# Kernel tuning notes

Hardware: AMD Instinct MI355X
Metric: run time of the kernel (lower is better)

Reference implementation:

```python
import jax, jax.numpy as jnp
import numpy as np

N_NODES = 100000
N_EDGES = 1600000
HID = 128
HEADS = 8
DK = HID // HEADS
N_LAYERS = 4
IN_DIM = 32
N_CLASSES = 16


def _ln(x, g, b, eps=1e-5):
    mu = x.mean(-1, keepdims=True)
    var = x.var(-1, keepdims=True)
    return (x - mu) / jnp.sqrt(var + eps) * g + b


def setup_inputs() -> dict:
    key = jax.random.key(0)
    ks = jax.random.split(key, 24)
    s = 0.05
    inp = {
        'feat': jax.random.randint(ks[0], (N_NODES,), 0, IN_DIM, dtype=jnp.int32),
        'edge_src': jax.random.randint(ks[1], (N_EDGES,), 0, N_NODES, dtype=jnp.int32),
        'edge_dst': jnp.sort(jax.random.randint(ks[2], (N_EDGES,), 0, N_NODES, dtype=jnp.int32)),
        'emb': jax.random.normal(ks[3], (IN_DIM, HID), jnp.float32) * s,
        'Wq': jax.random.normal(ks[4], (N_LAYERS, HID, HID), jnp.float32) * s,
        'Wk': jax.random.normal(ks[5], (N_LAYERS, HID, HID), jnp.float32) * s,
        'Wv': jax.random.normal(ks[6], (N_LAYERS, HID, HID), jnp.float32) * s,
        'Wo': jax.random.normal(ks[7], (N_LAYERS, HID, HID), jnp.float32) * s,
        'bo': jnp.zeros((N_LAYERS, HID), jnp.float32),
        'ln1_g': jnp.ones((N_LAYERS, HID), jnp.float32),
        'ln1_b': jnp.zeros((N_LAYERS, HID), jnp.float32),
        'W1': jax.random.normal(ks[8], (N_LAYERS, HID, 2 * HID), jnp.float32) * s,
        'b1': jnp.zeros((N_LAYERS, 2 * HID), jnp.float32),
        'W2': jax.random.normal(ks[9], (N_LAYERS, 2 * HID, HID), jnp.float32) * s,
        'b2': jnp.zeros((N_LAYERS, HID), jnp.float32),
        'ln2_g': jnp.ones((N_LAYERS, HID), jnp.float32),
        'ln2_b': jnp.zeros((N_LAYERS, HID), jnp.float32),
        'mW0': jax.random.normal(ks[10], (HID, HID // 2), jnp.float32) * s,
        'mb0': jnp.zeros((HID // 2,), jnp.float32),
        'mW1': jax.random.normal(ks[11], (HID // 2, HID // 4), jnp.float32) * s,
        'mb1': jnp.zeros((HID // 4,), jnp.float32),
        'mW2': jax.random.normal(ks[12], (HID // 4, N_CLASSES), jnp.float32) * s,
        'mb2': jnp.zeros((N_CLASSES,), jnp.float32),
    }
    return inp


def reference(feat, edge_src, edge_dst, emb, Wq, Wk, Wv, Wo, bo, ln1_g, ln1_b,
              W1, b1, W2, b2, ln2_g, ln2_b, mW0, mb0, mW1, mb1, mW2, mb2):
    N = feat.shape[0]
    h = emb[feat]  # [N, HID] embedding gather
    inv_sqrt_dk = jnp.float32(1.0 / np.sqrt(DK))
    for l in range(Wq.shape[0]):
        h_in1 = h
        q = (h @ Wq[l]).reshape(N, HEADS, DK)
        k = (h @ Wk[l]).reshape(N, HEADS, DK)
        v = (h @ Wv[l]).reshape(N, HEADS, DK)
        # per-edge scores: K[src] . Q[dst], scaled, clipped, exponentiated
        sc = jnp.einsum('ehd,ehd->eh', k[edge_src], q[edge_dst]) * inv_sqrt_dk
        sc = jnp.exp(jnp.clip(sc, -5.0, 5.0))  # [E, HEADS]
        wV = jax.ops.segment_sum(sc[:, :, None] * v[edge_src], edge_dst, num_segments=N)
        z = jax.ops.segment_sum(sc, edge_dst, num_segments=N)
        attn = (wV / (z[:, :, None] + 1e-6)).reshape(N, HID)
        h = h_in1 + (attn @ Wo[l] + bo[l])  # residual + O proj
        h = _ln(h, ln1_g[l], ln1_b[l])
        h_in2 = h
        f = jax.nn.relu(h @ W1[l] + b1[l]) @ W2[l] + b2[l]
        h = _ln(h_in2 + f, ln2_g[l], ln2_b[l])
    # MLPReadout: HID -> HID/2 -> HID/4 -> n_classes
    h = jax.nn.relu(h @ mW0 + mb0)
    h = jax.nn.relu(h @ mW1 + mb1)
    return h @ mW2 + mb2
```

## Files before the change

kernel.cpp:

```cpp
#include <hip/hip_runtime.h>
#include <hip/hip_fp16.h>

#define HID 128
#define N_LAYERS 4
#define IN_DIM 32
#define N_CLASSES 16

typedef _Float16 f16x8 __attribute__((ext_vector_type(8)));
typedef float f32x2 __attribute__((ext_vector_type(2)));
typedef __attribute__((ext_vector_type(4))) float f32x4;
typedef unsigned int uint_t;

#if defined(__has_builtin)
#if __has_builtin(__builtin_amdgcn_cvt_pk_f32_fp8)
#define HAVE_CVT_FP8 1
#endif
#if __has_builtin(__builtin_amdgcn_cvt_pk_fp8_f32)
#define HAVE_ENC_FP8 1
#endif
#endif

__device__ __forceinline__ unsigned short f2bf(float f) {
    unsigned int u = __float_as_uint(f);
    return (unsigned short)((u + 0x7FFFu + ((u >> 16) & 1u)) >> 16);
}
__device__ __forceinline__ float2 up16(uint_t u) {
    __half2 h = *(__half2*)&u;
    return __half22float2(h);
}

__device__ __forceinline__ unsigned char f2e4m3(float f) {
    unsigned int u = __float_as_uint(f);
    unsigned char s = (unsigned char)((u >> 24) & 0x80u);
    unsigned int a = u & 0x7FFFFFFFu;
    if (a >= 0x43E00000u) return s | 0x7Eu;
    int exp = (int)(a >> 23) - 127;
    if (exp < -6) {
        int m = (int)rintf(__uint_as_float(a) * 512.f);
        return s | (unsigned char)m;
    }
    unsigned int lsb = (a >> 20) & 1u;
    a += 0x7FFFFu + lsb;
    int e8 = ((int)(a >> 23) - 127) + 7;
    unsigned int m8 = (a >> 20) & 7u;
    return s | (unsigned char)((e8 << 3) | (int)m8);
}
__device__ __forceinline__ float e4m32f(unsigned int b) {
    unsigned int s = (b & 0x80u) << 24;
    unsigned int E = (b >> 3) & 15u, m = b & 7u;
    if (E == 0) {
        float v = (float)m * 0.001953125f;
        return __uint_as_float(__float_as_uint(v) | s);
    }
    return __uint_as_float(s | ((E + 120u) << 23) | (m << 20));
}
__device__ __forceinline__ unsigned char enc8(float v) {
#ifdef HAVE_ENC_FP8
    int r = __builtin_amdgcn_cvt_pk_fp8_f32(v, v, 0, false);
    return (unsigned char)(r & 0xFF);
#else
    return f2e4m3(v);
#endif
}
__device__ __forceinline__ void dec8v(uint_t u, f32x2* o) {
#ifdef HAVE_CVT_FP8
    o[0] = __builtin_amdgcn_cvt_pk_f32_fp8(u, false);
    o[1] = __builtin_amdgcn_cvt_pk_f32_fp8(u, true);
#else
    o[0] = (f32x2){e4m32f(u & 255u), e4m32f((u >> 8) & 255u)};
    o[1] = (f32x2){e4m32f((u >> 16) & 255u), e4m32f(u >> 24)};
#endif
}

__global__ void detect_kernel(const unsigned int* __restrict__ ln1g, int* __restrict__ flag) {
    if (threadIdx.x == 0 && blockIdx.x == 0)
        *flag = (ln1g[0] == 0x3F800000u) ? 0 : 1;
}

#define NSM 11
struct SArgs {
    const void* src[NSM];
    float*      dst[NSM];
    int         cnt[NSM];
};

__global__ void conv_kernel(SArgs args, const int* __restrict__ flag) {
    int p = blockIdx.y;
    int n = args.cnt[p];
    int base = (blockIdx.x * 256 + threadIdx.x) * 4;
    if (base >= n) return;
    float* dst = args.dst[p];
    if (*flag) {
        const unsigned short* s = (const unsigned short*)args.src[p];
        #pragma unroll
        for (int j = 0; j < 4; ++j)
            dst[base + j] = __uint_as_float(((unsigned int)s[base + j]) << 16);
    } else {
        const float* s = (const float*)args.src[p];
        *(float4*)&dst[base] = *(const float4*)&s[base];
    }
}

#define NW 27
struct WArgs {
    const void* src[NW];
    int         soff[NW];
    _Float16*   dst[NW];
    int         K[NW];
    int         M[NW];
};

__global__ void wconv_kernel(WArgs a, const int* __restrict__ flag) {
    int p = blockIdx.y;
    int K = a.K[p], M = a.M[p];
    int idx = blockIdx.x * 256 + threadIdx.x;
    if (idx >= K * M) return;
    int k = idx / M, m = idx % M;
    float v;
    if (*flag)
        v = __uint_as_float(((unsigned int)((const unsigned short*)a.src[p])[a.soff[p] + idx]) << 16);
    else
        v = ((const float*)a.src[p])[a.soff[p] + idx];
    a.dst[p][(size_t)m * K + k] = (_Float16)v;
}

__global__ void csr_kernel(const int* __restrict__ dst, int* __restrict__ row_start,
                           int N, int E) {
    int n = blockIdx.x * 256 + threadIdx.x;
    if (n > N) return;
    int lo = 0, hi = E;
    while (lo < hi) {
        int mid = (lo + hi) >> 1;
        if (dst[mid] < n) lo = mid + 1; else hi = mid;
    }
    row_start[n] = lo;
}

__global__ void embed_kernel(const int* __restrict__ feat, const float* __restrict__ emb,
                             _Float16* __restrict__ h, int N) {
    int idx = blockIdx.x * 256 + threadIdx.x;
    if (idx >= N * 16) return;
    int n  = idx >> 4;
    int c8 = idx & 15;
    int f = feat[n];
    const float* s = &emb[(size_t)f * HID + c8 * 8];
    float4 a = *(const float4*)s;
    float4 b = *(const float4*)(s + 4);
    f16x8 o;
    o[0] = (_Float16)a.x; o[1] = (_Float16)a.y; o[2] = (_Float16)a.z; o[3] = (_Float16)a.w;
    o[4] = (_Float16)b.x; o[5] = (_Float16)b.y; o[6] = (_Float16)b.z; o[7] = (_Float16)b.w;
    *(f16x8*)&h[(size_t)n * HID + c8 * 8] = o;
}

template<int K, int KC, int MC>
__launch_bounds__(256)
__global__ void mfma_gemm_qkv(const _Float16* __restrict__ Ain,
                              const _Float16* __restrict__ Bt,
                              _Float16* __restrict__ q16, unsigned char* __restrict__ kvp8) {
    constexpr int NT  = MC / 16;
    constexpr int SAB = KC * 2 + 16;

    __shared__ __align__(16) char As[64 * SAB];
    __shared__ __align__(16) char Bs[MC * SAB];

    const int t    = threadIdx.x;
    const int w    = t >> 6;
    const int l    = t & 63;
    const int quad = l >> 4;
    const int lc   = l & 15;
    const int row0 = blockIdx.x * 64;
    const int mbase = blockIdx.y * MC;

    f32x4 acc[NT];
    #pragma unroll
    for (int i = 0; i < NT; ++i) acc[i] = (f32x4){0.f, 0.f, 0.f, 0.f};

    {
        constexpr int AU = 64 * KC / 8;
        #pragma unroll
        for (int i = 0; i < (AU + 255) / 256; ++i) {
            int idx = t + i * 256;
            if ((AU % 256 == 0) || idx < AU) {
                int r = idx / (KC / 8), u = idx % (KC / 8);
                *(uint4*)&As[r * SAB + u * 16] =
                    *(const uint4*)(Ain + (size_t)(row0 + r) * K + u * 8);
            }
        }
        constexpr int BU = MC * KC / 8;
        #pragma unroll
        for (int i = 0; i < (BU + 255) / 256; ++i) {
            int idx = t + i * 256;
            if ((BU % 256 == 0) || idx < BU) {
                int m = idx / (KC / 8), u = idx % (KC / 8);
                *(uint4*)&Bs[m * SAB + u * 16] =
                    *(const uint4*)(Bt + (size_t)(mbase + m) * K + u * 8);
            }
        }
        __syncthreads();
        #pragma unroll
        for (int kk = 0; kk < KC / 32; ++kk) {
            f16x8 af = *(const f16x8*)&As[(w * 16 + lc) * SAB + kk * 64 + quad * 16];
            #pragma unroll
            for (int i = 0; i < NT; ++i) {
                f16x8 bf = *(const f16x8*)&Bs[(i * 16 + lc) * SAB + kk * 64 + quad * 16];
                acc[i] = __builtin_amdgcn_mfma_f32_16x16x32_f16(af, bf, acc[i], 0, 0, 0);
            }
        }
    }

    #pragma unroll
    for (int r = 0; r < 4; ++r) {
        int row = row0 + w * 16 + quad * 4 + r;
        #pragma unroll
        for (int i = 0; i < NT; ++i) {
            float v = acc[i][r];
            int gc = mbase + i * 16 + lc;
            if (gc < 128)      q16[(size_t)row * 128 + gc] = (_Float16)v;
            else if (gc < 256) kvp8[(size_t)row * 256 + (gc - 128)] = enc8(v);
            else               kvp8[(size_t)row * 256 + 128 + (gc - 256)] = enc8(v);
        }
    }
}

template<int NEXTM, bool RMODE>
__launch_bounds__(256)
__global__ void layer_tail_fused(const _Float16* __restrict__ t2, _Float16* __restrict__ h,
                                 const _Float16* __restrict__ Wo, const _Float16* __restrict__ W1,
                                 const _Float16* __restrict__ W2,
                                 const _Float16* __restrict__ Wn, const float* __restrict__ bn,
                                 const float* __restrict__ bo,  const float* __restrict__ l1g,
                                 const float* __restrict__ l1b, const float* __restrict__ b1,
                                 const float* __restrict__ b2,  const float* __restrict__ l2g,
                                 const float* __restrict__ l2b,
                                 _Float16* __restrict__ q16, unsigned char* __restrict__ kvp8) {
    constexpr int SAB = 272;
    __shared__ __align__(16) char bufA[64 * SAB];
    __shared__ __align__(16) char bufT[64 * SAB];
    __shared__ __align__(16) char bufH[64 * SAB];
    __shared__ __align__(16) char bufB[64 * SAB];

    const int t    = threadIdx.x;
    const int w    = t >> 6;
    const int l    = t & 63;
    const int quad = l >> 4;
    const int lc   = l & 15;
    const int row0 = blockIdx.x * 64;
    const int arow = (w * 16 + lc) * SAB;

    #pragma unroll
    for (int i = 0; i < 4; ++i) {
        int idx = t + i * 256;
        int r = idx >> 4, u = idx & 15;
        *(uint4*)&bufA[r * SAB + u * 16] = *(const uint4*)(t2 + (size_t)(row0 + r) * 128 + u * 8);
        *(uint4*)&bufT[r * SAB + u * 16] = *(const uint4*)(h  + (size_t)(row0 + r) * 128 + u * 8);
    }

    f32x4 acc[8];
    #pragma unroll
    for (int i = 0; i < 8; ++i) acc[i] = (f32x4){0.f, 0.f, 0.f, 0.f};
    #pragma unroll
    for (int c = 0; c < 2; ++c) {
        if (c) __syncthreads();
        #pragma unroll
        for (int i = 0; i < 4; ++i) {
            int idx = t + i * 256;
            int r = idx >> 4, u = idx & 15;
            *(uint4*)&bufB[r * SAB + u * 16] = *(const uint4*)(Wo + (size_t)(c * 64 + r) * 128 + u * 8);
        }
        __syncthreads();
        #pragma unroll
        for (int kk = 0; kk < 4; ++kk) {
            f16x8 af = *(const f16x8*)&bufA[arow + kk * 64 + quad * 16];
            #pragma unroll
            for (int i = 0; i < 4; ++i) {
                f16x8 bf = *(const f16x8*)&bufB[(i * 16 + lc) * SAB + kk * 64 + quad * 16];
                acc[c * 4 + i] = __builtin_amdgcn_mfma_f32_16x16x32_f16(af, bf, acc[c * 4 + i], 0, 0, 0);
            }
        }
    }
    {
        float gv[8], bv[8], bb[8];
        #pragma unroll
        for (int j = 0; j < 8; ++j) {
            int col = j * 16 + lc;
            gv[j] = l1g[col]; bv[j] = l1b[col]; bb[j] = bo[col];
        }
        #pragma unroll
        for (int r = 0; r < 4; ++r) {
            int lrow = (w * 16 + quad * 4 + r) * SAB;
            float v[8];
            float s = 0.f, ss = 0.f;
            #pragma unroll
            for (int j = 0; j < 8; ++j) {
                float res = (float)*(const _Float16*)&bufT[lrow + (j * 16 + lc) * 2];
                v[j] = acc[j][r] + bb[j] + res;
                s += v[j]; ss += v[j] * v[j];
            }
            #pragma unroll
            for (int m = 1; m <= 8; m <<= 1) { s += __shfl_xor(s, m); ss += __shfl_xor(ss, m); }
            float mu   = s * (1.f / 128.f);
            float rstd = rsqrtf(ss * (1.f / 128.f) - mu * mu + 1e-5f);
            #pragma unroll
            for (int j = 0; j < 8; ++j) {
                float o = (v[j] - mu) * rstd * gv[j] + bv[j];
                *(_Float16*)&bufH[lrow + (j * 16 + lc) * 2] = (_Float16)o;
            }
        }
    }

    #pragma unroll
    for (int c = 0; c < 4; ++c) {
        __syncthreads();
        #pragma unroll
        for (int i = 0; i < 4; ++i) {
            int idx = t + i * 256;
            int r = idx >> 4, u = idx & 15;
            *(uint4*)&bufB[r * SAB + u * 16] = *(const uint4*)(W1 + (size_t)(c * 64 + r) * 128 + u * 8);
        }
        __syncthreads();
        f32x4 a2[4];
        #pragma unroll
        for (int i = 0; i < 4; ++i) a2[i] = (f32x4){0.f, 0.f, 0.f, 0.f};
        #pragma unroll
        for (int kk = 0; kk < 4; ++kk) {
            f16x8 af = *(const f16x8*)&bufH[arow + kk * 64 + quad * 16];
            #pragma unroll
            for (int i = 0; i < 4; ++i) {
                f16x8 bf = *(const f16x8*)&bufB[(i * 16 + lc) * SAB + kk * 64 + quad * 16];
                a2[i] = __builtin_amdgcn_mfma_f32_16x16x32_f16(af, bf, a2[i], 0, 0, 0);
            }
        }
        char* plane = (c < 2) ? bufA : bufT;
        const int cbyte = (c & 1) * 128;
        #pragma unroll
        for (int r = 0; r < 4; ++r) {
            int lrow = (w * 16 + quad * 4 + r) * SAB;
            #pragma unroll
            for (int i = 0; i < 4; ++i) {
                float v = a2[i][r] + b1[c * 64 + i * 16 + lc];
                v = fmaxf(v, 0.f);
                *(_Float16*)&plane[lrow + cbyte + (i * 16 + lc) * 2] = (_Float16)v;
            }
        }
    }

    f32x4 acc3[8];
    #pragma unroll
    for (int i = 0; i < 8; ++i) acc3[i] = (f32x4){0.f, 0.f, 0.f, 0.f};
    #pragma unroll
    for (int cc = 0; cc < 2; ++cc) {
        #pragma unroll
        for (int kh = 0; kh < 2; ++kh) {
            __syncthreads();
            #pragma unroll
            for (int i = 0; i < 4; ++i) {
                int idx = t + i * 256;
                int r = idx >> 4, u = idx & 15;
                *(uint4*)&bufB[r * SAB + u * 16] =
                    *(const uint4*)(W2 + (size_t)(cc * 64 + r) * 256 + kh * 128 + u * 8);
            }
            __syncthreads();
            const char* Ap = kh ? bufT : bufA;
            #pragma unroll
            for (int kk = 0; kk < 4; ++kk) {
                f16x8 af = *(const f16x8*)&Ap[arow + kk * 64 + quad * 16];
                #pragma unroll
                for (int i = 0; i < 4; ++i) {
                    f16x8 bf = *(const f16x8*)&bufB[(i * 16 + lc) * SAB + kk * 64 + quad * 16];
                    acc3[cc * 4 + i] = __builtin_amdgcn_mfma_f32_16x16x32_f16(af, bf, acc3[cc * 4 + i], 0, 0, 0);
                }
            }
        }
    }
    {
        float gv[8], bv[8], bb[8];
        #pragma unroll
        for (int j = 0; j < 8; ++j) {
            int col = j * 16 + lc;
            gv[j] = l2g[col]; bv[j] = l2b[col]; bb[j] = b2[col];
        }
        #pragma unroll
        for (int r = 0; r < 4; ++r) {
            int row = row0 + w * 16 + quad * 4 + r;
            int lrow = (w * 16 + quad * 4 + r) * SAB;
            float v[8];
            float s = 0.f, ss = 0.f;
            #pragma unroll
            for (int j = 0; j < 8; ++j) {
                float res = (float)*(const _Float16*)&bufH[lrow + (j * 16 + lc) * 2];
                v[j] = acc3[j][r] + bb[j] + res;
                s += v[j]; ss += v[j] * v[j];
            }
            #pragma unroll
            for (int m = 1; m <= 8; m <<= 1) { s += __shfl_xor(s, m); ss += __shfl_xor(ss, m); }
            float mu   = s * (1.f / 128.f);
            float rstd = rsqrtf(ss * (1.f / 128.f) - mu * mu + 1e-5f);
            #pragma unroll
            for (int j = 0; j < 8; ++j) {
                float o = (v[j] - mu) * rstd * gv[j] + bv[j];
                h[(size_t)row * 128 + j * 16 + lc] = (_Float16)o;
                *(_Float16*)&bufA[lrow + (j * 16 + lc) * 2] = (_Float16)o;
            }
        }
    }

    #pragma unroll
    for (int c = 0; c < NEXTM / 64; ++c) {
        __syncthreads();
        #pragma unroll
        for (int i = 0; i < 4; ++i) {
            int idx = t + i * 256;
            int r = idx >> 4, u = idx & 15;
            *(uint4*)&bufB[r * SAB + u * 16] = *(const uint4*)(Wn + (size_t)(c * 64 + r) * 128 + u * 8);
        }
        __syncthreads();
        f32x4 a4[4];
        #pragma unroll
        for (int i = 0; i < 4; ++i) a4[i] = (f32x4){0.f, 0.f, 0.f, 0.f};
        #pragma unroll
        for (int kk = 0; kk < 4; ++kk) {
            f16x8 af = *(const f16x8*)&bufA[arow + kk * 64 + quad * 16];
            #pragma unroll
            for (int i = 0; i < 4; ++i) {
                f16x8 bf = *(const f16x8*)&bufB[(i * 16 + lc) * SAB + kk * 64 + quad * 16];
                a4[i] = __builtin_amdgcn_mfma_f32_16x16x32_f16(af, bf, a4[i], 0, 0, 0);
            }
        }
        #pragma unroll
        for (int r = 0; r < 4; ++r) {
            int row = row0 + w * 16 + quad * 4 + r;
            #pragma unroll
            for (int i = 0; i < 4; ++i) {
                int gc = c * 64 + i * 16 + lc;
                float v = a4[i][r];
                if (RMODE) {
                    v += bn[gc];
                    v = fmaxf(v, 0.f);
                    q16[(size_t)row * 64 + gc] = (_Float16)v;
                } else {
                    if (gc < 128)      q16[(size_t)row * 128 + gc] = (_Float16)v;
                    else if (gc < 256) kvp8[(size_t)row * 256 + (gc - 128)] = enc8(v);
                    else               kvp8[(size_t)row * 256 + 128 + (gc - 256)] = enc8(v);
                }
            }
        }
    }
}

__launch_bounds__(256)
__global__ void readout_tail(const _Float16* __restrict__ r0,
                             const _Float16* __restrict__ w1t, const float* __restrict__ b1_,
                             const _Float16* __restrict__ w2t, const float* __restrict__ b2_,
                             void* __restrict__ outp, const int* __restrict__ flag, int N) {
    constexpr int SA = 144;
    constexpr int SR = 80;
    __shared__ __align__(16) char bufA[64 * SA];
    __shared__ __align__(16) char bufR[64 * SR];

    const int t    = threadIdx.x;
    const int w    = t >> 6;
    const int l    = t & 63;
    const int quad = l >> 4;
    const int lc   = l & 15;
    const int row0 = blockIdx.x * 64;

    #pragma unroll
    for (int i = 0; i < 2; ++i) {
        int idx = t + i * 256;
        int r = idx >> 3, u = idx & 7;
        *(uint4*)&bufA[r * SA + u * 16] = *(const uint4*)(r0 + (size_t)(row0 + r) * 64 + u * 8);
    }
    __syncthreads();

    f32x4 acc[2];
    acc[0] = (f32x4){0.f, 0.f, 0.f, 0.f};
    acc[1] = (f32x4){0.f, 0.f, 0.f, 0.f};
    #pragma unroll
    for (int kk = 0; kk < 2; ++kk) {
        f16x8 af = *(const f16x8*)&bufA[(w * 16 + lc) * SA + kk * 64 + quad * 16];
        #pragma unroll
        for (int i = 0; i < 2; ++i) {
            f16x8 bf = *(const f16x8*)(w1t + (size_t)(i * 16 + lc) * 64 + kk * 32 + quad * 8);
            acc[i] = __builtin_amdgcn_mfma_f32_16x16x32_f16(af, bf, acc[i], 0, 0, 0);
        }
    }
    #pragma unroll
    for (int r = 0; r < 4; ++r) {
        int lrow = (w * 16 + quad * 4 + r) * SR;
        #pragma unroll
        for (int i = 0; i < 2; ++i) {
            float v = acc[i][r] + b1_[i * 16 + lc];
            v = fmaxf(v, 0.f);
            *(_Float16*)&bufR[lrow + (i * 16 + lc) * 2] = (_Float16)v;
        }
    }
    f32x4 a2 = (f32x4){0.f, 0.f, 0.f, 0.f};
    {
        f16x8 af = *(const f16x8*)&bufR[(w * 16 + lc) * SR + quad * 16];
        f16x8 bf = *(const f16x8*)(w2t + (size_t)lc * 32 + quad * 8);
        a2 = __builtin_amdgcn_mfma_f32_16x16x32_f16(af, bf, a2, 0, 0, 0);
    }
    #pragma unroll
    for (int r = 0; r < 4; ++r) {
        int row = row0 + w * 16 + quad * 4 + r;
        if (row < N) {
            float v = a2[r] + b2_[lc];
            size_t o = (size_t)row * 16 + lc;
            if (*flag) ((unsigned short*)outp)[o] = f2bf(v);
            else       ((float*)outp)[o] = v;
        }
    }
}

__global__ void attn_kernel(const _Float16* __restrict__ q16, const uint_t* __restrict__ kvp,
                            const int* __restrict__ esrc, const int* __restrict__ rows,
                            _Float16* __restrict__ out, int N) {
    int node = (blockIdx.x * blockDim.x + threadIdx.x) >> 6;
    if (node >= N) return;
    int l    = threadIdx.x & 63;
    int head = l & 7;
    int eg   = l >> 3;

    f32x2 qh[8];
    {
        const uint4* qp = (const uint4*)(q16 + (size_t)node * HID + head * 16);
        uint4 q0 = qp[0], q1 = qp[1];
        uint_t qs[8] = {q0.x, q0.y, q0.z, q0.w, q1.x, q1.y, q1.z, q1.w};
        #pragma unroll
        for (int i = 0; i < 8; ++i) {
            float2 f = up16(qs[i]);
            qh[i] = (f32x2){f.x * 0.25f, f.y * 0.25f};
        }
    }
    int e0 = rows[node], e1 = rows[node + 1];
    f32x2 wv[8];
    #pragma unroll
    for (int i = 0; i < 8; ++i) wv[i] = (f32x2){0.f, 0.f};
    float z = 0.f;

    for (int eb = e0; eb < e1; eb += 16) {
        int ea = eb + eg, ec = eb + 8 + eg;
        bool oka = ea < e1, okc = ec < e1;
        int sa  = esrc[oka ? ea : e1 - 1];
        int sc_ = esrc[okc ? ec : e1 - 1];
        uint4 ka = *(const uint4*)(kvp + (size_t)sa  * 64 + head * 4);
        uint4 va = *(const uint4*)(kvp + (size_t)sa  * 64 + 32 + head * 4);
        uint4 kc = *(const uint4*)(kvp + (size_t)sc_ * 64 + head * 4);
        uint4 vc = *(const uint4*)(kvp + (size_t)sc_ * 64 + 32 + head * 4);

        f32x2 k2a[8], k2c[8];
        dec8v(ka.x, k2a); dec8v(ka.y, k2a + 2); dec8v(ka.z, k2a + 4); dec8v(ka.w, k2a + 6);
        dec8v(kc.x, k2c); dec8v(kc.y, k2c + 2); dec8v(kc.z, k2c + 4); dec8v(kc.w, k2c + 6);
        f32x2 da2 = (f32x2){0.f, 0.f}, dc2 = (f32x2){0.f, 0.f};
        #pragma unroll
        for (int j = 0; j < 8; ++j) { da2 += qh[j] * k2a[j]; dc2 += qh[j] * k2c[j]; }
        float da = da2.x + da2.y, dc = dc2.x + dc2.y;
        float sa2 = oka ? __expf(fminf(fmaxf(da, -5.f), 5.f)) : 0.f;
        float sc2 = okc ? __expf(fminf(fmaxf(dc, -5.f), 5.f)) : 0.f;

        f32x2 v2a[8], v2c[8];
        dec8v(va.x, v2a); dec8v(va.y, v2a + 2); dec8v(va.z, v2a + 4); dec8v(va.w, v2a + 6);
        dec8v(vc.x, v2c); dec8v(vc.y, v2c + 2); dec8v(vc.z, v2c + 4); dec8v(vc.w, v2c + 6);
        f32x2 pa = (f32x2){sa2, sa2}, pc = (f32x2){sc2, sc2};
        #pragma unroll
        for (int j = 0; j < 8; ++j) { wv[j] += pa * v2a[j]; wv[j] += pc * v2c[j]; }
        z += sa2 + sc2;
    }
    #pragma unroll
    for (int m = 8; m < 64; m <<= 1) {
        z += __shfl_xor(z, m);
        #pragma unroll
        for (int i = 0; i < 8; ++i) {
            wv[i].x += __shfl_xor(wv[i].x, m);
            wv[i].y += __shfl_xor(wv[i].y, m);
        }
    }
    if (eg == 0) {
        float inv = 1.f / (z + 1e-6f);
        f16x8 o0, o1;
        #pragma unroll
        for (int i = 0; i < 4; ++i) {
            o0[2*i]   = (_Float16)(wv[i].x * inv);
            o0[2*i+1] = (_Float16)(wv[i].y * inv);
            o1[2*i]   = (_Float16)(wv[4+i].x * inv);
            o1[2*i+1] = (_Float16)(wv[4+i].y * inv);
        }
        *(f16x8*)&out[(size_t)node * HID + head * 16]     = o0;
        *(f16x8*)&out[(size_t)node * HID + head * 16 + 8] = o1;
    }
}

extern "C" void kernel_launch(void* const* d_in, const int* in_sizes, int n_in,
                              void* d_out, int out_size, void* d_ws, size_t ws_size,
                              hipStream_t stream) {
    const int N  = in_sizes[0];
    const int E  = in_sizes[1];
    const int RB = (N + 63) / 64;
    const size_t NP = (size_t)RB * 64;

    const int* d_feat = (const int*)d_in[0];
    const int* d_esrc = (const int*)d_in[1];
    const int* d_edst = (const int*)d_in[2];

    char* base = (char*)d_ws;
    size_t cur = 0;
    auto alloc = [&](size_t bytes) -> char* {
        cur = (cur + 255) & ~(size_t)255;
        char* p = base + cur;
        cur += bytes;
        return p;
    };
    int* d_flag = (int*)alloc(4);
    int* d_rows = (int*)alloc((size_t)(N + 1) * 4);

    float* p_emb = (float*)alloc(IN_DIM * HID * 4);
    float* p_bo  = (float*)alloc(N_LAYERS * HID * 4);
    float* p_l1g = (float*)alloc(N_LAYERS * HID * 4);
    float* p_l1b = (float*)alloc(N_LAYERS * HID * 4);
    float* p_b1  = (float*)alloc(N_LAYERS * 2 * HID * 4);
    float* p_b2  = (float*)alloc(N_LAYERS * HID * 4);
    float* p_l2g = (float*)alloc(N_LAYERS * HID * 4);
    float* p_l2b = (float*)alloc(N_LAYERS * HID * 4);
    float* p_mb0 = (float*)alloc(64 * 4);
    float* p_mb1 = (float*)alloc(32 * 4);
    float* p_mb2 = (float*)alloc(16 * 4);

    _Float16* wqkv_t = (_Float16*)alloc((size_t)N_LAYERS * 384 * 128 * 2);
    _Float16* wo_t   = (_Float16*)alloc((size_t)N_LAYERS * 128 * 128 * 2);
    _Float16* w1_t   = (_Float16*)alloc((size_t)N_LAYERS * 256 * 128 * 2);
    _Float16* w2_t   = (_Float16*)alloc((size_t)N_LAYERS * 128 * 256 * 2);
    _Float16* mw0_t  = (_Float16*)alloc(64 * 128 * 2);
    _Float16* mw1_t  = (_Float16*)alloc(32 * 64 * 2);
    _Float16* mw2_t  = (_Float16*)alloc(16 * 32 * 2);

    _Float16*      buf_h = (_Float16*)alloc(NP * HID * 2);
    _Float16*      q16   = (_Float16*)alloc(NP * HID * 2);
    _Float16*      t2    = (_Float16*)alloc(NP * HID * 2);
    unsigned char* kvp   = (unsigned char*)alloc(NP * 256);

    detect_kernel<<<1, 64, 0, stream>>>((const unsigned int*)d_in[9], d_flag);

    {
        SArgs sa;
        const int sidx[NSM] = {3, 8, 9, 10, 12, 14, 15, 16, 18, 20, 22};
        float*    sdst[NSM] = {p_emb, p_bo, p_l1g, p_l1b, p_b1, p_b2, p_l2g, p_l2b, p_mb0, p_mb1, p_mb2};
        const int scnt[NSM] = {IN_DIM*HID, N_LAYERS*HID, N_LAYERS*HID, N_LAYERS*HID,
                               N_LAYERS*2*HID, N_LAYERS*HID, N_LAYERS*HID, N_LAYERS*HID, 64, 32, 16};
        for (int i = 0; i < NSM; ++i) { sa.src[i] = d_in[sidx[i]]; sa.dst[i] = sdst[i]; sa.cnt[i] = scnt[i]; }
        conv_kernel<<<dim3(4, NSM), 256, 0, stream>>>(sa, d_flag);
    }

    {
        WArgs wa;
        int wi = 0;
        auto addw = [&](int inp, int off, int Kd, int Md, _Float16* dst) {
            wa.src[wi] = d_in[inp]; wa.soff[wi] = off; wa.K[wi] = Kd; wa.M[wi] = Md;
            wa.dst[wi] = dst; ++wi;
        };
        for (int l = 0; l < N_LAYERS; ++l) {
            addw(4,  l * 16384, 128, 128, wqkv_t + (size_t)l * 49152);
            addw(5,  l * 16384, 128, 128, wqkv_t + (size_t)l * 49152 + 16384);
            addw(6,  l * 16384, 128, 128, wqkv_t + (size_t)l * 49152 + 32768);
            addw(7,  l * 16384, 128, 128, wo_t + (size_t)l * 16384);
            addw(11, l * 32768, 128, 256, w1_t + (size_t)l * 32768);
            addw(13, l * 32768, 256, 128, w2_t + (size_t)l * 32768);
        }
        addw(17, 0, 128, 64, mw0_t);
        addw(19, 0, 64,  32, mw1_t);
        addw(21, 0, 32,  16, mw2_t);
        wconv_kernel<<<dim3(128, NW), 256, 0, stream>>>(wa, d_flag);
    }

    csr_kernel<<<(N + 1 + 255) / 256, 256, 0, stream>>>(d_edst, d_rows, N, E);
    embed_kernel<<<((size_t)N * 16 + 255) / 256, 256, 0, stream>>>(d_feat, p_emb, buf_h, N);

    const int GBW = (N + 3) / 4;

    mfma_gemm_qkv<128, 128, 192><<<dim3(RB, 2), 256, 0, stream>>>(buf_h, wqkv_t, q16, kvp);

    for (int l = 0; l < N_LAYERS; ++l) {
        const _Float16* Wo = wo_t + (size_t)l * 16384;
        const _Float16* W1 = w1_t + (size_t)l * 32768;
        const _Float16* W2 = w2_t + (size_t)l * 32768;
        const float* bo  = p_bo  + (size_t)l * HID;
        const float* l1g = p_l1g + (size_t)l * HID;
        const float* l1b = p_l1b + (size_t)l * HID;
        const float* b1  = p_b1  + (size_t)l * 2 * HID;
        const float* b2  = p_b2  + (size_t)l * HID;
        const float* l2g = p_l2g + (size_t)l * HID;
        const float* l2b = p_l2b + (size_t)l * HID;

        attn_kernel<<<GBW, 256, 0, stream>>>(q16, (const uint_t*)kvp, d_esrc, d_rows, t2, N);

        if (l < N_LAYERS - 1) {
            layer_tail_fused<384, false><<<RB, 256, 0, stream>>>(
                t2, buf_h, Wo, W1, W2, wqkv_t + (size_t)(l + 1) * 49152, nullptr,
                bo, l1g, l1b, b1, b2, l2g, l2b, q16, kvp);
        } else {
            layer_tail_fused<64, true><<<RB, 256, 0, stream>>>(
                t2, buf_h, Wo, W1, W2, mw0_t, p_mb0,
                bo, l1g, l1b, b1, b2, l2g, l2b, q16, nullptr);
        }
    }

    readout_tail<<<RB, 256, 0, stream>>>(q16, mw1_t, p_mb1, mw2_t, p_mb2, d_out, d_flag, N);
}
```

Measured before the change: 842.6 us.

## Load GEMM B operands directly from global into registers, drop LDS weight staging

Weight tiles for the QKV GEMM and the fused layer-tail GEMMs are now read straight from global memory (L2-resident) into registers with one-tile-ahead prefetch, instead of being staged through a shared-memory buffer. This removes the bufB LDS buffer and the __syncthreads pairs around each weight load. The activation loads are reorganised so each wave fills only its own rows, and launch bounds request 3 blocks per CU. The QKV kernel becomes a single-dimension grid computing all 384 columns per block. The cost is that every wave re-reads the weights from cache, with more global traffic and register pressure.

Measured after the change: 1.335 ms. 1.58x slower.

```diff
diff --git a/kernel.cpp b/kernel.cpp
--- a/kernel.cpp
+++ b/kernel.cpp
@@ -152,78 +152,72 @@
     *(f16x8*)&h[(size_t)n * HID + c8 * 8] = o;
 }
 
-template<int K, int KC, int MC>
-__launch_bounds__(256)
+template<int NT>
+__device__ __forceinline__ void gemm128_gB(const char* Arow, const _Float16* Bt,
+                                           int colstride, int lc, int quad, f32x4* acc) {
+    uint4 cur[4], nxt[4];
+    const _Float16* p0 = Bt + (size_t)lc * colstride + quad * 8;
+    #pragma unroll
+    for (int kk = 0; kk < 4; ++kk) cur[kk] = *(const uint4*)(p0 + kk * 32);
+    #pragma unroll
+    for (int i = 0; i < NT; ++i) {
+        if (i + 1 < NT) {
+            const _Float16* p = p0 + (size_t)(i + 1) * 16 * colstride;
+            #pragma unroll
+            for (int kk = 0; kk < 4; ++kk) nxt[kk] = *(const uint4*)(p + kk * 32);
+        }
+        #pragma unroll
+        for (int kk = 0; kk < 4; ++kk) {
+            f16x8 af = *(const f16x8*)(Arow + kk * 64 + quad * 16);
+            acc[i] = __builtin_amdgcn_mfma_f32_16x16x32_f16(af, *(const f16x8*)&cur[kk],
+                                                            acc[i], 0, 0, 0);
+        }
+        #pragma unroll
+        for (int kk = 0; kk < 4; ++kk) cur[kk] = nxt[kk];
+    }
+}
+
+__launch_bounds__(256, 3)
 __global__ void mfma_gemm_qkv(const _Float16* __restrict__ Ain,
                               const _Float16* __restrict__ Bt,
                               _Float16* __restrict__ q16, unsigned char* __restrict__ kvp8) {
-    constexpr int NT  = MC / 16;
-    constexpr int SAB = KC * 2 + 16;
-
+    constexpr int SAB = 272;
     __shared__ __align__(16) char As[64 * SAB];
-    __shared__ __align__(16) char Bs[MC * SAB];
-
-    const int t    = threadIdx.x;
-    const int w    = t >> 6;
-    const int l    = t & 63;
-    const int quad = l >> 4;
-    const int lc   = l & 15;
+    const int t = threadIdx.x, w = t >> 6, l = t & 63;
+    const int quad = l >> 4, lc = l & 15;
     const int row0 = blockIdx.x * 64;
-    const int mbase = blockIdx.y * MC;
-
-    f32x4 acc[NT];
-    #pragma unroll
-    for (int i = 0; i < NT; ++i) acc[i] = (f32x4){0.f, 0.f, 0.f, 0.f};
-
-    {
-        constexpr int AU = 64 * KC / 8;
-        #pragma unroll
-        for (int i = 0; i < (AU + 255) / 256; ++i) {
-            int idx = t + i * 256;
-            if ((AU % 256 == 0) || idx < AU) {
-                int r = idx / (KC / 8), u = idx % (KC / 8);
-                *(uint4*)&As[r * SAB + u * 16] =
-                    *(const uint4*)(Ain + (size_t)(row0 + r) * K + u * 8);
+    const int arow = (w * 16 + lc) * SAB;
+
+    #pragma unroll
+    for (int i = 0; i < 4; ++i) {
+        int idx = i * 64 + l;
+        int rr = idx >> 4, u = idx & 15;
+        *(uint4*)&As[(w * 16 + rr) * SAB + u * 16] =
+            *(const uint4*)(Ain + (size_t)(row0 + w * 16 + rr) * 128 + u * 8);
+    }
+    #pragma unroll
+    for (int c = 0; c < 6; ++c) {
+        f32x4 acc[4];
+        #pragma unroll
+        for (int i = 0; i < 4; ++i) acc[i] = (f32x4){0.f, 0.f, 0.f, 0.f};
+        gemm128_gB<4>(As + arow, Bt + (size_t)c * 64 * 128, 128, lc, quad, acc);
+        #pragma unroll
+        for (int r = 0; r < 4; ++r) {
+            int row = row0 + w * 16 + quad * 4 + r;
+            #pragma unroll
+            for (int i = 0; i < 4; ++i) {
+                float v = acc[i][r];
+                int gc = c * 64 + i * 16 + lc;
+                if (gc < 128)      q16[(size_t)row * 128 + gc] = (_Float16)v;
+                else if (gc < 256) kvp8[(size_t)row * 256 + (gc - 128)] = enc8(v);
+                else               kvp8[(size_t)row * 256 + 128 + (gc - 256)] = enc8(v);
             }
         }
-        constexpr int BU = MC * KC / 8;
-        #pragma unroll
-        for (int i = 0; i < (BU + 255) / 256; ++i) {
-            int idx = t + i * 256;
-            if ((BU % 256 == 0) || idx < BU) {
-                int m = idx / (KC / 8), u = idx % (KC / 8);
-                *(uint4*)&Bs[m * SAB + u * 16] =
-                    *(const uint4*)(Bt + (size_t)(mbase + m) * K + u * 8);
-            }
-        }
-        __syncthreads();
-        #pragma unroll
-        for (int kk = 0; kk < KC / 32; ++kk) {
-            f16x8 af = *(const f16x8*)&As[(w * 16 + lc) * SAB + kk * 64 + quad * 16];
-            #pragma unroll
-            for (int i = 0; i < NT; ++i) {
-                f16x8 bf = *(const f16x8*)&Bs[(i * 16 + lc) * SAB + kk * 64 + quad * 16];
-                acc[i] = __builtin_amdgcn_mfma_f32_16x16x32_f16(af, bf, acc[i], 0, 0, 0);
-            }
-        }
-    }
-
-    #pragma unroll
-    for (int r = 0; r < 4; ++r) {
-        int row = row0 + w * 16 + quad * 4 + r;
-        #pragma unroll
-        for (int i = 0; i < NT; ++i) {
-            float v = acc[i][r];
-            int gc = mbase + i * 16 + lc;
-            if (gc < 128)      q16[(size_t)row * 128 + gc] = (_Float16)v;
-            else if (gc < 256) kvp8[(size_t)row * 256 + (gc - 128)] = enc8(v);
-            else               kvp8[(size_t)row * 256 + 128 + (gc - 256)] = enc8(v);
-        }
     }
 }
 
 template<int NEXTM, bool RMODE>
-__launch_bounds__(256)
+__launch_bounds__(256, 3)
 __global__ void layer_tail_fused(const _Float16* __restrict__ t2, _Float16* __restrict__ h,
                                  const _Float16* __restrict__ Wo, const _Float16* __restrict__ W1,
                                  const _Float16* __restrict__ W2,
@@ -237,47 +231,26 @@
     __shared__ __align__(16) char bufA[64 * SAB];
     __shared__ __align__(16) char bufT[64 * SAB];
     __shared__ __align__(16) char bufH[64 * SAB];
-    __shared__ __align__(16) char bufB[64 * SAB];
-
-    const int t    = threadIdx.x;
-    const int w    = t >> 6;
-    const int l    = t & 63;
-    const int quad = l >> 4;
-    const int lc   = l & 15;
+
+    const int t = threadIdx.x, w = t >> 6, l = t & 63;
+    const int quad = l >> 4, lc = l & 15;
     const int row0 = blockIdx.x * 64;
     const int arow = (w * 16 + lc) * SAB;
 
     #pragma unroll
     for (int i = 0; i < 4; ++i) {
-        int idx = t + i * 256;
-        int r = idx >> 4, u = idx & 15;
-        *(uint4*)&bufA[r * SAB + u * 16] = *(const uint4*)(t2 + (size_t)(row0 + r) * 128 + u * 8);
-        *(uint4*)&bufT[r * SAB + u * 16] = *(const uint4*)(h  + (size_t)(row0 + r) * 128 + u * 8);
+        int idx = i * 64 + l;
+        int rr = idx >> 4, u = idx & 15;
+        int grow = row0 + w * 16 + rr;
+        *(uint4*)&bufA[(w * 16 + rr) * SAB + u * 16] = *(const uint4*)(t2 + (size_t)grow * 128 + u * 8);
+        *(uint4*)&bufT[(w * 16 + rr) * SAB + u * 16] = *(const uint4*)(h  + (size_t)grow * 128 + u * 8);
     }
 
     f32x4 acc[8];
     #pragma unroll
     for (int i = 0; i < 8; ++i) acc[i] = (f32x4){0.f, 0.f, 0.f, 0.f};
-    #pragma unroll
-    for (int c = 0; c < 2; ++c) {
-        if (c) __syncthreads();
-        #pragma unroll
-        for (int i = 0; i < 4; ++i) {
-            int idx = t + i * 256;
-            int r = idx >> 4, u = idx & 15;
-            *(uint4*)&bufB[r * SAB + u * 16] = *(const uint4*)(Wo + (size_t)(c * 64 + r) * 128 + u * 8);
-        }
-        __syncthreads();
-        #pragma unroll
-        for (int kk = 0; kk < 4; ++kk) {
-            f16x8 af = *(const f16x8*)&bufA[arow + kk * 64 + quad * 16];
-            #pragma unroll
-            for (int i = 0; i < 4; ++i) {
-                f16x8 bf = *(const f16x8*)&bufB[(i * 16 + lc) * SAB + kk * 64 + quad * 16];
-                acc[c * 4 + i] = __builtin_amdgcn_mfma_f32_16x16x32_f16(af, bf, acc[c * 4 + i], 0, 0, 0);
-            }
-        }
-    }
+    gemm128_gB<8>(bufA + arow, Wo, 128, lc, quad, acc);
+
     {
         float gv[8], bv[8], bb[8];
         #pragma unroll
@@ -310,26 +283,10 @@
 
     #pragma unroll
     for (int c = 0; c < 4; ++c) {
-        __syncthreads();
-        #pragma unroll
-        for (int i = 0; i < 4; ++i) {
-            int idx = t + i * 256;
-            int r = idx >> 4, u = idx & 15;
-            *(uint4*)&bufB[r * SAB + u * 16] = *(const uint4*)(W1 + (size_t)(c * 64 + r) * 128 + u * 8);
-        }
-        __syncthreads();
         f32x4 a2[4];
         #pragma unroll
         for (int i = 0; i < 4; ++i) a2[i] = (f32x4){0.f, 0.f, 0.f, 0.f};
-        #pragma unroll
-        for (int kk = 0; kk < 4; ++kk) {
-            f16x8 af = *(const f16x8*)&bufH[arow + kk * 64 + quad * 16];
-            #pragma unroll
-            for (int i = 0; i < 4; ++i) {
-                f16x8 bf = *(const f16x8*)&bufB[(i * 16 + lc) * SAB + kk * 64 + quad * 16];
-                a2[i] = __builtin_amdgcn_mfma_f32_16x16x32_f16(af, bf, a2[i], 0, 0, 0);
-            }
-        }
+        gemm128_gB<4>(bufH + arow, W1 + (size_t)c * 64 * 128, 128, lc, quad, a2);
         char* plane = (c < 2) ? bufA : bufT;
         const int cbyte = (c & 1) * 128;
         #pragma unroll
@@ -349,28 +306,8 @@
     for (int i = 0; i < 8; ++i) acc3[i] = (f32x4){0.f, 0.f, 0.f, 0.f};
     #pragma unroll
     for (int cc = 0; cc < 2; ++cc) {
-        #pragma unroll
-        for (int kh = 0; kh < 2; ++kh) {
-            __syncthreads();
-            #pragma unroll
-            for (int i = 0; i < 4; ++i) {
-                int idx = t + i * 256;
-                int r = idx >> 4, u = idx & 15;
-                *(uint4*)&bufB[r * SAB + u * 16] =
-                    *(const uint4*)(W2 + (size_t)(cc * 64 + r) * 256 + kh * 128 + u * 8);
-            }
-            __syncthreads();
-            const char* Ap = kh ? bufT : bufA;
-            #pragma unroll
-            for (int kk = 0; kk < 4; ++kk) {
-                f16x8 af = *(const f16x8*)&Ap[arow + kk * 64 + quad * 16];
-                #pragma unroll
-                for (int i = 0; i < 4; ++i) {
-                    f16x8 bf = *(const f16x8*)&bufB[(i * 16 + lc) * SAB + kk * 64 + quad * 16];
-                    acc3[cc * 4 + i] = __builtin_amdgcn_mfma_f32_16x16x32_f16(af, bf, acc3[cc * 4 + i], 0, 0, 0);
-                }
-            }
-        }
+        gemm128_gB<4>(bufA + arow, W2 + (size_t)cc * 64 * 256,       256, lc, quad, acc3 + cc * 4);
+        gemm128_gB<4>(bufT + arow, W2 + (size_t)cc * 64 * 256 + 128, 256, lc, quad, acc3 + cc * 4);
     }
     {
         float gv[8], bv[8], bb[8];
@@ -406,26 +343,10 @@
 
     #pragma unroll
     for (int c = 0; c < NEXTM / 64; ++c) {
-        __syncthreads();
-        #pragma unroll
-        for (int i = 0; i < 4; ++i) {
-            int idx = t + i * 256;
-            int r = idx >> 4, u = idx & 15;
-            *(uint4*)&bufB[r * SAB + u * 16] = *(const uint4*)(Wn + (size_t)(c * 64 + r) * 128 + u * 8);
-        }
-        __syncthreads();
         f32x4 a4[4];
         #pragma unroll
         for (int i = 0; i < 4; ++i) a4[i] = (f32x4){0.f, 0.f, 0.f, 0.f};
-        #pragma unroll
-        for (int kk = 0; kk < 4; ++kk) {
-            f16x8 af = *(const f16x8*)&bufA[arow + kk * 64 + quad * 16];
-            #pragma unroll
-            for (int i = 0; i < 4; ++i) {
-                f16x8 bf = *(const f16x8*)&bufB[(i * 16 + lc) * SAB + kk * 64 + quad * 16];
-                a4[i] = __builtin_amdgcn_mfma_f32_16x16x32_f16(af, bf, a4[i], 0, 0, 0);
-            }
-        }
+        gemm128_gB<4>(bufA + arow, Wn + (size_t)c * 64 * 128, 128, lc, quad, a4);
         #pragma unroll
         for (int r = 0; r < 4; ++r) {
             int row = row0 + w * 16 + quad * 4 + r;
@@ -676,7 +597,7 @@
 
     const int GBW = (N + 3) / 4;
 
-    mfma_gemm_qkv<128, 128, 192><<<dim3(RB, 2), 256, 0, stream>>>(buf_h, wqkv_t, q16, kvp);
+    mfma_gemm_qkv<<<RB, 256, 0, stream>>>(buf_h, wqkv_t, q16, kvp);
 
     for (int l = 0; l < N_LAYERS; ++l) {
         const _Float16* Wo = wo_t + (size_t)l * 16384;
```

## Drop bufT shared buffer by holding residual in registers and interleaving FFN halves

Applied to the files above, without the earlier changes.

The residual h is now loaded directly into registers instead of a shared staging buffer, and the FFN is reorganized so each 128-wide half of the hidden activation is computed into bufA and immediately consumed by the matching W2 slice. This removes one 17KB LDS buffer (four down to three), which should let more blocks reside per CU. It adds per-lane scalar global loads for the residual (strided, less coalesced) and keeps 32 extra half values in registers, which may raise register pressure.

New measurement: 841.0 us (median of 2 runs). About the same (-0.2%).

```diff
diff --git a/kernel.cpp b/kernel.cpp
--- a/kernel.cpp
+++ b/kernel.cpp
@@ -235,49 +235,62 @@
                                  _Float16* __restrict__ q16, unsigned char* __restrict__ kvp8) {
     constexpr int SAB = 272;
     __shared__ __align__(16) char bufA[64 * SAB];
-    __shared__ __align__(16) char bufT[64 * SAB];
     __shared__ __align__(16) char bufH[64 * SAB];
     __shared__ __align__(16) char bufB[64 * SAB];
 
-    const int t    = threadIdx.x;
-    const int w    = t >> 6;
-    const int l    = t & 63;
-    const int quad = l >> 4;
-    const int lc   = l & 15;
+    const int t = threadIdx.x, w = t >> 6, l = t & 63;
+    const int quad = l >> 4, lc = l & 15;
     const int row0 = blockIdx.x * 64;
     const int arow = (w * 16 + lc) * SAB;
+
+    _Float16 resv[4][8];
+    #pragma unroll
+    for (int r = 0; r < 4; ++r) {
+        int row = row0 + w * 16 + quad * 4 + r;
+        #pragma unroll
+        for (int j = 0; j < 8; ++j)
+            resv[r][j] = h[(size_t)row * 128 + j * 16 + lc];
+    }
 
     #pragma unroll
     for (int i = 0; i < 4; ++i) {
         int idx = t + i * 256;
         int r = idx >> 4, u = idx & 15;
         *(uint4*)&bufA[r * SAB + u * 16] = *(const uint4*)(t2 + (size_t)(row0 + r) * 128 + u * 8);
-        *(uint4*)&bufT[r * SAB + u * 16] = *(const uint4*)(h  + (size_t)(row0 + r) * 128 + u * 8);
-    }
-
-    f32x4 acc[8];
-    #pragma unroll
-    for (int i = 0; i < 8; ++i) acc[i] = (f32x4){0.f, 0.f, 0.f, 0.f};
-    #pragma unroll
-    for (int c = 0; c < 2; ++c) {
-        if (c) __syncthreads();
+    }
+
+    auto stageW = [&](const _Float16* src, int rowStride) {
+        __syncthreads();
         #pragma unroll
         for (int i = 0; i < 4; ++i) {
             int idx = t + i * 256;
             int r = idx >> 4, u = idx & 15;
-            *(uint4*)&bufB[r * SAB + u * 16] = *(const uint4*)(Wo + (size_t)(c * 64 + r) * 128 + u * 8);
+            *(uint4*)&bufB[r * SAB + u * 16] =
+                *(const uint4*)(src + (size_t)r * rowStride + u * 8);
         }
         __syncthreads();
+    };
+    auto mf4 = [&](const char* Ar, f32x4* acc) {
         #pragma unroll
         for (int kk = 0; kk < 4; ++kk) {
-            f16x8 af = *(const f16x8*)&bufA[arow + kk * 64 + quad * 16];
+            f16x8 af = *(const f16x8*)(Ar + kk * 64 + quad * 16);
             #pragma unroll
             for (int i = 0; i < 4; ++i) {
                 f16x8 bf = *(const f16x8*)&bufB[(i * 16 + lc) * SAB + kk * 64 + quad * 16];
-                acc[c * 4 + i] = __builtin_amdgcn_mfma_f32_16x16x32_f16(af, bf, acc[c * 4 + i], 0, 0, 0);
-            }
-        }
-    }
+                acc[i] = __builtin_amdgcn_mfma_f32_16x16x32_f16(af, bf, acc[i], 0, 0, 0);
+            }
+        }
+    };
+
+    f32x4 acc[8];
+    #pragma unroll
+    for (int i = 0; i < 8; ++i) acc[i] = (f32x4){0.f, 0.f, 0.f, 0.f};
+    #pragma unroll
+    for (int c = 0; c < 2; ++c) {
+        stageW(Wo + (size_t)c * 64 * 128, 128);
+        mf4(bufA + arow, acc + c * 4);
+    }
+
     {
         float gv[8], bv[8], bb[8];
         #pragma unroll
@@ -292,8 +305,7 @@
             float s = 0.f, ss = 0.f;
             #pragma unroll
             for (int j = 0; j < 8; ++j) {
-                float res = (float)*(const _Float16*)&bufT[lrow + (j * 16 + lc) * 2];
-                v[j] = acc[j][r] + bb[j] + res;
+                v[j] = acc[j][r] + bb[j] + (float)resv[r][j];
                 s += v[j]; ss += v[j] * v[j];
             }
             #pragma unroll
@@ -308,70 +320,37 @@
         }
     }
 
-    #pragma unroll
-    for (int c = 0; c < 4; ++c) {
-        __syncthreads();
-        #pragma unroll
-        for (int i = 0; i < 4; ++i) {
-            int idx = t + i * 256;
-            int r = idx >> 4, u = idx & 15;
-            *(uint4*)&bufB[r * SAB + u * 16] = *(const uint4*)(W1 + (size_t)(c * 64 + r) * 128 + u * 8);
-        }
-        __syncthreads();
-        f32x4 a2[4];
-        #pragma unroll
-        for (int i = 0; i < 4; ++i) a2[i] = (f32x4){0.f, 0.f, 0.f, 0.f};
-        #pragma unroll
-        for (int kk = 0; kk < 4; ++kk) {
-            f16x8 af = *(const f16x8*)&bufH[arow + kk * 64 + quad * 16];
-            #pragma unroll
-            for (int i = 0; i < 4; ++i) {
-                f16x8 bf = *(const f16x8*)&bufB[(i * 16 + lc) * SAB + kk * 64 + quad * 16];
-                a2[i] = __builtin_amdgcn_mfma_f32_16x16x32_f16(af, bf, a2[i], 0, 0, 0);
-            }
-        }
-        char* plane = (c < 2) ? bufA : bufT;
-        const int cbyte = (c & 1) * 128;
-        #pragma unroll
-        for (int r = 0; r < 4; ++r) {
-            int lrow = (w * 16 + quad * 4 + r) * SAB;
-            #pragma unroll
-            for (int i = 0; i < 4; ++i) {
-                float v = a2[i][r] + b1[c * 64 + i * 16 + lc];
-                v = fmaxf(v, 0.f);
-                *(_Float16*)&plane[lrow + cbyte + (i * 16 + lc) * 2] = (_Float16)v;
-            }
-        }
-    }
-
     f32x4 acc3[8];
     #pragma unroll
     for (int i = 0; i < 8; ++i) acc3[i] = (f32x4){0.f, 0.f, 0.f, 0.f};
     #pragma unroll
-    for (int cc = 0; cc < 2; ++cc) {
-        #pragma unroll
-        for (int kh = 0; kh < 2; ++kh) {
-            __syncthreads();
-            #pragma unroll
-            for (int i = 0; i < 4; ++i) {
-                int idx = t + i * 256;
-                int r = idx >> 4, u = idx & 15;
-                *(uint4*)&bufB[r * SAB + u * 16] =
-                    *(const uint4*)(W2 + (size_t)(cc * 64 + r) * 256 + kh * 128 + u * 8);
-            }
-            __syncthreads();
-            const char* Ap = kh ? bufT : bufA;
-            #pragma unroll
-            for (int kk = 0; kk < 4; ++kk) {
-                f16x8 af = *(const f16x8*)&Ap[arow + kk * 64 + quad * 16];
+    for (int half = 0; half < 2; ++half) {
+        #pragma unroll
+        for (int c2 = 0; c2 < 2; ++c2) {
+            int c = half * 2 + c2;
+            stageW(W1 + (size_t)c * 64 * 128, 128);
+            f32x4 a2[4];
+            #pragma unroll
+            for (int i = 0; i < 4; ++i) a2[i] = (f32x4){0.f, 0.f, 0.f, 0.f};
+            mf4(bufH + arow, a2);
+            #pragma unroll
+            for (int r = 0; r < 4; ++r) {
+                int lrow = (w * 16 + quad * 4 + r) * SAB;
                 #pragma unroll
                 for (int i = 0; i < 4; ++i) {
-                    f16x8 bf = *(const f16x8*)&bufB[(i * 16 + lc) * SAB + kk * 64 + quad * 16];
-                    acc3[cc * 4 + i] = __builtin_amdgcn_mfma_f32_16x16x32_f16(af, bf, acc3[cc * 4 + i], 0, 0, 0);
+                    float v = a2[i][r] + b1[c * 64 + i * 16 + lc];
+                    v = fmaxf(v, 0.f);
+                    *(_Float16*)&bufA[lrow + c2 * 128 + (i * 16 + lc) * 2] = (_Float16)v;
                 }
             }
         }
-    }
+        #pragma unroll
+        for (int cc = 0; cc < 2; ++cc) {
+            stageW(W2 + (size_t)cc * 64 * 256 + half * 128, 256);
+            mf4(bufA + arow, acc3 + cc * 4);
+        }
+    }
+
     {
         float gv[8], bv[8], bb[8];
         #pragma unroll
@@ -406,26 +385,11 @@
 
     #pragma unroll
     for (int c = 0; c < NEXTM / 64; ++c) {
-        __syncthreads();
-        #pragma unroll
-        for (int i = 0; i < 4; ++i) {
-            int idx = t + i * 256;
-            int r = idx >> 4, u = idx & 15;
-            *(uint4*)&bufB[r * SAB + u * 16] = *(const uint4*)(Wn + (size_t)(c * 64 + r) * 128 + u * 8);
-        }
-        __syncthreads();
+        stageW(Wn + (size_t)c * 64 * 128, 128);
         f32x4 a4[4];
         #pragma unroll
         for (int i = 0; i < 4; ++i) a4[i] = (f32x4){0.f, 0.f, 0.f, 0.f};
-        #pragma unroll
-        for (int kk = 0; kk < 4; ++kk) {
-            f16x8 af = *(const f16x8*)&bufA[arow + kk * 64 + quad * 16];
-            #pragma unroll
-            for (int i = 0; i < 4; ++i) {
-                f16x8 bf = *(const f16x8*)&bufB[(i * 16 + lc) * SAB + kk * 64 + quad * 16];
-                a4[i] = __builtin_amdgcn_mfma_f32_16x16x32_f16(af, bf, a4[i], 0, 0, 0);
-            }
-        }
+        mf4(bufA + arow, a4);
         #pragma unroll
         for (int r = 0; r < 4; ++r) {
             int row = row0 + w * 16 + quad * 4 + r;
```
